# Performance work log

Hardware: AMD Instinct MI355X
Metric: run time of the kernel (lower is better)

Reference implementation:

```python
import jax, jax.numpy as jnp
import numpy as np

B, T, V = 128, 1024, 192
EPS = 1e-8


def setup_inputs() -> dict:
    key = jax.random.key(0)
    k1, k2, k3, k4, k5 = jax.random.split(key, 5)
    return {
        "emissions": jax.random.normal(k1, (B, T, V), dtype=jnp.float32),
        "tags": jax.random.randint(k2, (B, T), 0, V, dtype=jnp.int64),
        "mask": jnp.ones((B, T), dtype=jnp.int32),
        "transitions": jax.random.normal(k3, (V, V), dtype=jnp.float32) * 0.1,
        "start_trans": jax.random.normal(k4, (V,), dtype=jnp.float32) * 0.1,
        "end_trans": jax.random.normal(k5, (V,), dtype=jnp.float32) * 0.1,
    }


def _lse(x, axis):
    # matches torch _log_sum_exp: max + log(sum(exp(x-max)) + 1e-8)
    m = jnp.max(x, axis=axis)
    return m + jnp.log(jnp.sum(jnp.exp(x - jnp.expand_dims(m, axis)), axis=axis) + EPS)


def _log_partition(emissions, mask, transitions, start_trans, end_trans):
    # emissions: (B,T,V), mask: (B,T) int
    alpha0 = start_trans[None, :] + emissions[:, 0, :]  # (B,V)
    em_t = jnp.moveaxis(emissions[:, 1:, :], 1, 0)       # (T-1,B,V)
    mk_t = jnp.moveaxis(mask[:, 1:], 1, 0).astype(bool)  # (T-1,B)

    def step(alpha, inp):
        emit, m = inp  # (B,V), (B,)
        # (B, V_prev, V_next)
        scores = alpha[:, :, None] + transitions[None, :, :] + emit[:, None, :]
        new_alpha = _lse(scores, axis=1)
        alpha = jnp.where(m[:, None], new_alpha, alpha)
        return alpha, None

    alpha, _ = jax.lax.scan(step, alpha0, (em_t, mk_t))
    return _lse(alpha + end_trans[None, :], axis=1)  # (B,)


def _gold_score(emissions, tags, mask, transitions, start_trans, end_trans):
    Bq, Tq, _ = emissions.shape
    maskf = mask.astype(emissions.dtype)
    # emission score of gold tags at each step: (B,T)
    emit = jnp.take_along_axis(emissions, tags[:, :, None], axis=2)[:, :, 0]
    # transitions between consecutive gold tags: (B,T-1)
    trans = transitions[tags[:, :-1], tags[:, 1:]]
    score = start_trans[tags[:, 0]] + emit[:, 0]
    score = score + jnp.sum((emit[:, 1:] + trans) * maskf[:, 1:], axis=1)
    last_idx = jnp.sum(mask, axis=1).astype(jnp.int32) - 1  # (B,)
    last_tags = jnp.take_along_axis(tags, last_idx[:, None].astype(tags.dtype), axis=1)[:, 0]
    score = score + end_trans[last_tags]
    return score


def reference(emissions, tags, mask, transitions, start_trans, end_trans):
    log_den = _log_partition(emissions, mask, transitions, start_trans, end_trans)
    log_num = _gold_score(emissions, tags, mask, transitions, start_trans, end_trans)
    raw_loss = log_den - log_num
    seq_len = jnp.clip(jnp.sum(mask, axis=1).astype(emissions.dtype), 1.0)
    return raw_loss / seq_len  # (B,)
```

## Files before the change

kernel.cpp:

```cpp
#include <hip/hip_runtime.h>

#define BB 128
#define TT 1024
#define VV 192
#define NTHREADS 256
#define NWAVES 4
#define LN2 0.69314718055994530942f
#define WS_STRIDE 448

typedef int   intx8   __attribute__((ext_vector_type(8)));
typedef float floatx2 __attribute__((ext_vector_type(2)));
typedef float floatx4 __attribute__((ext_vector_type(4)));

__device__ __forceinline__ float bf8_to_f32(unsigned char h) {
    floatx2 v = __builtin_amdgcn_cvt_pk_f32_bf8((int)(unsigned int)h, false);
    return v.x;
}
__device__ __forceinline__ unsigned char f32_to_bf8(float f) {
    int pk = __builtin_amdgcn_cvt_pk_bf8_f32(f, f, 0, false);
    return (unsigned char)(pk & 0xff);
}
__device__ __forceinline__ unsigned char f32_to_fp8(float f) {
    int pk = __builtin_amdgcn_cvt_pk_fp8_f32(f, f, 0, false);
    return (unsigned char)(pk & 0xff);
}

#define LBAR() __asm__ volatile("s_waitcnt lgkmcnt(0)\n\ts_barrier" ::: "memory")

template<int DIR>
__device__ __forceinline__ void crf_body(const float* __restrict__ emissions,
                                         const int* __restrict__ tags,
                                         const int* __restrict__ mask,
                                         const float* __restrict__ trans,
                                         const float* __restrict__ start_trans,
                                         const float* __restrict__ end_trans,
                                         float* __restrict__ ws)
{
    const int b = blockIdx.x;
    const int tid = threadIdx.x;
    const int lane = tid & 63;
    const int wid = tid >> 6;
    const int quad = lane >> 4;
    const int col = lane & 15;

    __shared__ __align__(16) unsigned char qpad[2][256];
    __shared__ unsigned int smaskp[33];
    __shared__ float wg[NWAVES];
    __shared__ float wsl[NWAVES];

    const float* em_b = emissions + (size_t)b * TT * VV;
    const int* mask_b = mask + b * TT;
    float* wsb = ws + (size_t)b * WS_STRIDE;

    const int nl = wid * 48 + (quad < 3 ? quad : 0) * 16 + col;

    #define ROWOF(u) (DIR ? (TT - 1 - (u)) : (u))

    intx8 ef[6];
    #pragma unroll
    for (int kt = 0; kt < 2; ++kt) {
        #pragma unroll
        for (int h = 0; h < 3; ++h) {
            const int n = wid * 48 + h * 16 + col;
            intx8 v;
            #pragma unroll
            for (int w = 0; w < 8; ++w) {
                unsigned int word = 0;
                #pragma unroll
                for (int by = 0; by < 4; ++by) {
                    int k = kt * 128 + quad * 32 + w * 4 + by;
                    float x = (k < VV) ? __expf(trans[DIR ? (k + n * VV) : (k * VV + n)]) : 0.f;
                    word |= (unsigned int)f32_to_fp8(x) << (8 * by);
                }
                v[w] = (int)word;
            }
            ef[kt * 3 + h] = v;
        }
    }

    for (int i = tid; i < 512; i += NTHREADS) ((unsigned char*)qpad)[i] = 0;

    if (tid < 33) {
        if (tid == 32) smaskp[32] = 0u;
        else {
            unsigned int m = 0;
            #pragma unroll 4
            for (int j = 0; j < 32; ++j) m |= (mask_b[tid * 32 + j] ? 1u : 0u) << j;
            smaskp[tid] = m;
        }
    }

    float em0[8], em1[8];
    #pragma unroll
    for (int r = 0; r < 8; ++r) em0[r] = em_b[(size_t)ROWOF(r) * VV + nl];
    #pragma unroll
    for (int r = 0; r < 8; ++r) em1[r] = em_b[(size_t)ROWOF(8 + r) * VV + nl];
    float em_fin = em_b[(size_t)ROWOF(512) * VV + nl];

    __syncthreads();
    if (tid < VV) {
        float a0 = DIR ? (end_trans[tid] + em_b[(size_t)(TT - 1) * VV + tid])
                       : (start_trans[tid] + em_b[tid]);
        qpad[0][tid] = f32_to_bf8(fminf(__expf(a0), 28672.f));
    }
    float carry2 = 0.f;
    int cur = 0;
    float peprev = __expf(em0[0]);
    __syncthreads();

    unsigned long long mk64 = 0; int boff = 0;
    auto fetchwin = [&](int u0w) {
        int wbase = DIR ? (TT - u0w - 16) : u0w;
        int mw = wbase >> 5;
        unsigned mlo = (unsigned)__builtin_amdgcn_readfirstlane((int)smaskp[mw]);
        unsigned mhi = (unsigned)__builtin_amdgcn_readfirstlane((int)smaskp[mw + 1]);
        mk64 = (((unsigned long long)mhi) << 32) | (unsigned long long)mlo;
        boff = wbase & 31;
    };
    auto getmk = [&](int i) -> int {
        int sh = DIR ? (boff + 16 - i) : (boff + i);
        return (int)((mk64 >> sh) & 1ull);
    };

    auto dostep = [&](float emraw, int mk) {
        unsigned char* qc = qpad[cur];
        const intx8* qv = (const intx8*)qc;
        intx8 A0 = qv[quad];
        intx8 A1 = qv[quad + 4];
        unsigned char prevb = 0;
        if (!mk) prevb = qc[nl];

        floatx4 aA[3], aB[3];
        #pragma unroll
        for (int h = 0; h < 3; ++h) { aA[h] = (floatx4){0.f,0.f,0.f,0.f};
                                      aB[h] = (floatx4){0.f,0.f,0.f,0.f}; }
        #pragma unroll
        for (int h = 0; h < 3; ++h)
            aA[h] = __builtin_amdgcn_mfma_scale_f32_16x16x128_f8f6f4(
                        A0, ef[h], aA[h], 1, 0, 0, 0x7f7f7f7f, 0, 0x7f7f7f7f);
        #pragma unroll
        for (int h = 0; h < 3; ++h)
            aB[h] = __builtin_amdgcn_mfma_scale_f32_16x16x128_f8f6f4(
                        A1, ef[3 + h], aB[h], 1, 0, 0, 0x7f7f7f7f, 0, 0x7f7f7f7f);

        int q0i = __builtin_amdgcn_readfirstlane(A0[0]);
        float q0 = bf8_to_f32((unsigned char)(q0i & 0xff));
        float r = __builtin_amdgcn_rcpf(q0);
        carry2 += mk ? __log2f(q0) : 0.f;
        float pe = __expf(emraw);
        float sc = pe * r;

        float s0 = aA[0][0] + aB[0][0];
        float s1 = aA[1][0] + aB[1][0];
        float s2 = aA[2][0] + aB[2][0];
        float v = (quad == 1) ? s1 : ((quad == 2) ? s2 : s0);
        float qn = fminf(v * sc, 28672.f);
        unsigned char nb;
        if (mk) {
            nb = f32_to_bf8(qn);
        } else {
            nb = DIR ? f32_to_bf8(fminf(bf8_to_f32(prevb) * pe *
                                        __builtin_amdgcn_rcpf(peprev), 28672.f))
                     : prevb;
        }
        qpad[cur ^ 1][nl] = nb;
        LBAR();
        cur ^= 1;
        if (DIR) peprev = pe;
    };

    for (int u0 = 0; u0 < 496; u0 += 16) {
        fetchwin(u0);
        if (u0 > 0) dostep(em0[0], getmk(0));
        dostep(em0[1], getmk(1));
        dostep(em0[2], getmk(2));
        dostep(em0[3], getmk(3));
        dostep(em0[4], getmk(4));
        dostep(em0[5], getmk(5));
        dostep(em0[6], getmk(6));
        dostep(em0[7], getmk(7));
        {
            #pragma unroll
            for (int r = 0; r < 8; ++r) {
                int rr = u0 + 16 + r;
                em0[r] = em_b[(size_t)ROWOF(rr) * VV + nl];
            }
        }
        dostep(em1[0], getmk(8));
        dostep(em1[1], getmk(9));
        dostep(em1[2], getmk(10));
        dostep(em1[3], getmk(11));
        dostep(em1[4], getmk(12));
        dostep(em1[5], getmk(13));
        dostep(em1[6], getmk(14));
        dostep(em1[7], getmk(15));
        {
            #pragma unroll
            for (int r = 0; r < 8; ++r) {
                int rr = u0 + 24 + r;
                em1[r] = em_b[(size_t)ROWOF(rr) * VV + nl];
            }
        }
    }
    fetchwin(496);
    dostep(em0[0], getmk(0)); dostep(em0[1], getmk(1));
    dostep(em0[2], getmk(2)); dostep(em0[3], getmk(3));
    dostep(em0[4], getmk(4)); dostep(em0[5], getmk(5));
    dostep(em0[6], getmk(6)); dostep(em0[7], getmk(7));
    dostep(em1[0], getmk(8)); dostep(em1[1], getmk(9));
    dostep(em1[2], getmk(10)); dostep(em1[3], getmk(11));
    dostep(em1[4], getmk(12)); dostep(em1[5], getmk(13));
    dostep(em1[6], getmk(14));

    if (DIR == 0) {
        dostep(em1[7], getmk(15));
        dostep(em_fin, getmk(16));
        if (tid < VV) wsb[tid] = bf8_to_f32(qpad[cur][tid]);
    } else {
        unsigned char* qc = qpad[cur];
        const intx8* qv = (const intx8*)qc;
        intx8 A0 = qv[quad];
        intx8 A1 = qv[quad + 4];
        int mk = (int)((smaskp[513 >> 5] >> (513 & 31)) & 1u);
        floatx4 aA[3], aB[3];
        #pragma unroll
        for (int h = 0; h < 3; ++h) { aA[h] = (floatx4){0.f,0.f,0.f,0.f};
                                      aB[h] = (floatx4){0.f,0.f,0.f,0.f}; }
        #pragma unroll
        for (int h = 0; h < 3; ++h)
            aA[h] = __builtin_amdgcn_mfma_scale_f32_16x16x128_f8f6f4(
                        A0, ef[h], aA[h], 1, 0, 0, 0x7f7f7f7f, 0, 0x7f7f7f7f);
        #pragma unroll
        for (int h = 0; h < 3; ++h)
            aB[h] = __builtin_amdgcn_mfma_scale_f32_16x16x128_f8f6f4(
                        A1, ef[3 + h], aB[h], 1, 0, 0, 0x7f7f7f7f, 0, 0x7f7f7f7f);
        if (quad < 3) {
            float s0 = aA[0][0] + aB[0][0];
            float s1 = aA[1][0] + aB[1][0];
            float s2 = aA[2][0] + aB[2][0];
            float v = (quad == 1) ? s1 : ((quad == 2) ? s2 : s0);
            if (!mk) v = bf8_to_f32(qc[nl]) * __builtin_amdgcn_rcpf(peprev);
            wsb[192 + nl] = v;
        }
    }
    if (tid == 0) wsb[384 + DIR] = carry2;

    float gp = 0.f;
    float sl = 0.f;
    for (int t = tid; t < TT; t += NTHREADS) {
        int mk = (int)((smaskp[t >> 5] >> (t & 31)) & 1u);
        bool inS = DIR ? (t >= 512) : (t < 512);
        if (inS) sl += (float)mk;
        bool inG = DIR ? (t >= 513) : (t >= 1 && t <= 512);
        if (inG) {
            int tg  = tags[b * TT + t];
            int tgp = tags[b * TT + t - 1];
            float term = em_b[(size_t)t * VV + tg] + trans[tgp * VV + tg];
            gp += mk ? term : 0.f;
        }
    }
    #pragma unroll
    for (int off = 1; off < 64; off <<= 1) {
        gp += __shfl_xor(gp, off);
        sl += __shfl_xor(sl, off);
    }
    if (lane == 0) { wg[wid] = gp; wsl[wid] = sl; }
    __syncthreads();
    if (tid == 0) {
        float g = 0.f, s = 0.f;
        for (int w = 0; w < NWAVES; ++w) { g += wg[w]; s += wsl[w]; }
        if (DIR == 0) {
            int tg0 = tags[b * TT];
            g += start_trans[tg0] + em_b[tg0];
        }
        wsb[386 + DIR] = g;
        wsb[388 + DIR] = s;
    }
    #undef ROWOF
}

__launch_bounds__(NTHREADS, 1)
__global__ void crf_half_kernel(const float* __restrict__ emissions,
                                const int* __restrict__ tags,
                                const int* __restrict__ mask,
                                const float* __restrict__ trans,
                                const float* __restrict__ start_trans,
                                const float* __restrict__ end_trans,
                                float* __restrict__ ws)
{
    if (blockIdx.y == 0)
        crf_body<0>(emissions, tags, mask, trans, start_trans, end_trans, ws);
    else
        crf_body<1>(emissions, tags, mask, trans, start_trans, end_trans, ws);
}

__global__ void crf_combine(const float* __restrict__ ws,
                            const int* __restrict__ tags,
                            const float* __restrict__ end_trans,
                            float* __restrict__ out)
{
    const int b = blockIdx.x;
    const int lane = threadIdx.x;
    const float* wsb = ws + (size_t)b * WS_STRIDE;
    float s = 0.f;
    #pragma unroll
    for (int i = lane; i < VV; i += 64) s += wsb[i] * wsb[192 + i];
    #pragma unroll
    for (int off = 1; off < 64; off <<= 1) s += __shfl_xor(s, off);
    if (lane == 0) {
        float logden = LN2 * (wsb[384] + wsb[385]) + __logf(s + 1e-8f);
        float gold = wsb[386] + wsb[387];
        int seqs = (int)(wsb[388] + wsb[389]);
        int last_idx = seqs - 1; if (last_idx < 0) last_idx = 0;
        gold += end_trans[tags[b * TT + last_idx]];
        float seqf = fmaxf((float)seqs, 1.0f);
        out[b] = (logden - gold) / seqf;
    }
}

extern "C" void kernel_launch(void* const* d_in, const int* in_sizes, int n_in,
                              void* d_out, int out_size, void* d_ws, size_t ws_size,
                              hipStream_t stream) {
    const float* emissions   = (const float*)d_in[0];
    const int*   tags        = (const int*)d_in[1];
    const int*   mask        = (const int*)d_in[2];
    const float* trans       = (const float*)d_in[3];
    const float* start_trans = (const float*)d_in[4];
    const float* end_trans   = (const float*)d_in[5];
    float* out = (float*)d_out;
    float* ws  = (float*)d_ws;

    crf_half_kernel<<<dim3(BB, 2), NTHREADS, 0, stream>>>(emissions, tags, mask, trans,
                                                          start_trans, end_trans, ws);
    crf_combine<<<BB, 64, 0, stream>>>(ws, tags, end_trans, out);
}
```

Baseline: 292.0 us.

## Split each half-sequence scan into four concurrent chunks with burn-in for ILP

Each 512-step directional scan is split into four chunks that run interleaved in one block. Chunks after the first start from a uniform vector and run a short burn-in, and the normalized state after burn-in is used to recover each chunk's log-scale contribution. This cuts the serial dependency chain from about 512 steps to about 144 rounds, with four independent MFMA chains per round hiding latency. In exchange each round does four times the work and shared memory, and the result relies on the forward-algorithm state forgetting its start (mixing) within the burn-in window, which is only approximately exact.

```diff
diff --git a/kernel.cpp b/kernel.cpp
--- a/kernel.cpp
+++ b/kernel.cpp
@@ -4,7 +4,6 @@
 #define TT 1024
 #define VV 192
 #define NTHREADS 256
-#define NWAVES 4
 #define LN2 0.69314718055994530942f
 #define WS_STRIDE 448
 
@@ -43,10 +42,9 @@
     const int quad = lane >> 4;
     const int col = lane & 15;
 
-    __shared__ __align__(16) unsigned char qpad[2][256];
+    __shared__ __align__(16) unsigned char qpad[4][2][256];
     __shared__ unsigned int smaskp[33];
-    __shared__ float wg[NWAVES];
-    __shared__ float wsl[NWAVES];
+    __shared__ float wgs[4], wsls[4];
 
     const float* em_b = emissions + (size_t)b * TT * VV;
     const int* mask_b = mask + b * TT;
@@ -54,7 +52,11 @@
 
     const int nl = wid * 48 + (quad < 3 ? quad : 0) * 16 + col;
 
-    #define ROWOF(u) (DIR ? (TT - 1 - (u)) : (u))
+    const int firstc[4] = {1, 113, 241, DIR ? 367 : 369};
+    const int capRc[4]  = {0, 16, 16, DIR ? 18 : 16};
+    const int capPc[4]  = {128, 144, 144, 0};
+
+    #define ROW_OF(x) (DIR ? (TT - 1 - (x)) : (x))
 
     intx8 ef[6];
     #pragma unroll
@@ -78,7 +80,7 @@
         }
     }
 
-    for (int i = tid; i < 512; i += NTHREADS) ((unsigned char*)qpad)[i] = 0;
+    for (int i = tid; i < 4 * 512; i += NTHREADS) ((unsigned char*)qpad)[i] = 0;
 
     if (tid < 33) {
         if (tid == 32) smaskp[32] = 0u;
@@ -90,163 +92,176 @@
         }
     }
 
-    float em0[8], em1[8];
-    #pragma unroll
-    for (int r = 0; r < 8; ++r) em0[r] = em_b[(size_t)ROWOF(r) * VV + nl];
-    #pragma unroll
-    for (int r = 0; r < 8; ++r) em1[r] = em_b[(size_t)ROWOF(8 + r) * VV + nl];
-    float em_fin = em_b[(size_t)ROWOF(512) * VV + nl];
+    float em0[4][8], em1[4][8];
+    #pragma unroll
+    for (int c = 0; c < 4; ++c) {
+        #pragma unroll
+        for (int r = 0; r < 8; ++r) em0[c][r] = em_b[(size_t)ROW_OF(firstc[c] + r) * VV + nl];
+        #pragma unroll
+        for (int r = 0; r < 8; ++r) em1[c][r] = em_b[(size_t)ROW_OF(firstc[c] + 8 + r) * VV + nl];
+    }
+    float pep[4] = {0.f, 0.f, 0.f, 0.f};
+    if (DIR) {
+        #pragma unroll
+        for (int c = 0; c < 4; ++c)
+            pep[c] = __expf(em_b[(size_t)ROW_OF(firstc[c] - 1) * VV + nl]);
+    }
 
     __syncthreads();
     if (tid < VV) {
         float a0 = DIR ? (end_trans[tid] + em_b[(size_t)(TT - 1) * VV + tid])
                        : (start_trans[tid] + em_b[tid]);
-        qpad[0][tid] = f32_to_bf8(fminf(__expf(a0), 28672.f));
-    }
-    float carry2 = 0.f;
+        qpad[0][0][tid] = f32_to_bf8(fminf(__expf(a0), 28672.f));
+        unsigned char one = f32_to_bf8(1.0f);
+        qpad[1][0][tid] = one;
+        qpad[2][0][tid] = one;
+        qpad[3][0][tid] = one;
+    }
+    float carry[4] = {0.f,0.f,0.f,0.f}, Rv[4] = {0.f,0.f,0.f,0.f};
+    float Pv[4] = {0.f,0.f,0.f,0.f}, csv[4] = {0.f,0.f,0.f,0.f};
     int cur = 0;
-    float peprev = __expf(em0[0]);
     __syncthreads();
 
-    unsigned long long mk64 = 0; int boff = 0;
-    auto fetchwin = [&](int u0w) {
-        int wbase = DIR ? (TT - u0w - 16) : u0w;
-        int mw = wbase >> 5;
-        unsigned mlo = (unsigned)__builtin_amdgcn_readfirstlane((int)smaskp[mw]);
-        unsigned mhi = (unsigned)__builtin_amdgcn_readfirstlane((int)smaskp[mw + 1]);
-        mk64 = (((unsigned long long)mhi) << 32) | (unsigned long long)mlo;
-        boff = wbase & 31;
-    };
-    auto getmk = [&](int i) -> int {
-        int sh = DIR ? (boff + 16 - i) : (boff + i);
-        return (int)((mk64 >> sh) & 1ull);
-    };
-
-    auto dostep = [&](float emraw, int mk) {
-        unsigned char* qc = qpad[cur];
-        const intx8* qv = (const intx8*)qc;
+    unsigned long long mk64[4];
+    int shb[4];
+
+#define GETMK(c, I) ((int)((mk64[c] >> (DIR ? (shb[c] + 15 - (I)) : (shb[c] + (I)))) & 1ull))
+
+#define ROUND(I)                                                               \
+    {                                                                          \
+        intx8 a0_[4], a1_[4];                                                  \
+        _Pragma("unroll")                                                      \
+        for (int c = 0; c < 4; ++c) {                                          \
+            const intx8* qv = (const intx8*)qpad[c][cur];                      \
+            a0_[c] = qv[quad];                                                 \
+            a1_[c] = qv[quad + 4];                                             \
+        }                                                                      \
+        floatx4 aA_[4][3], aB_[4][3];                                          \
+        _Pragma("unroll")                                                      \
+        for (int c = 0; c < 4; ++c) {                                          \
+            _Pragma("unroll")                                                  \
+            for (int h = 0; h < 3; ++h) {                                      \
+                floatx4 z = (floatx4){0.f, 0.f, 0.f, 0.f};                     \
+                aA_[c][h] = __builtin_amdgcn_mfma_scale_f32_16x16x128_f8f6f4(  \
+                    a0_[c], ef[h], z, 1, 0, 0, 0x7f7f7f7f, 0, 0x7f7f7f7f);     \
+                aB_[c][h] = __builtin_amdgcn_mfma_scale_f32_16x16x128_f8f6f4(  \
+                    a1_[c], ef[3 + h], z, 1, 0, 0, 0x7f7f7f7f, 0, 0x7f7f7f7f); \
+            }                                                                  \
+        }                                                                      \
+        _Pragma("unroll")                                                      \
+        for (int c = 0; c < 4; ++c) {                                          \
+            int mk = GETMK(c, I);                                              \
+            unsigned char prevb = 0;                                           \
+            if (!mk) prevb = qpad[c][cur][nl];                                 \
+            int q0i = __builtin_amdgcn_readfirstlane(a0_[c][0]);               \
+            float q0 = bf8_to_f32((unsigned char)(q0i & 0xff));                \
+            float rr = __builtin_amdgcn_rcpf(q0);                              \
+            carry[c] += mk ? __log2f(q0) : 0.f;                                \
+            float emraw = ((I) < 8) ? em0[c][(I) & 7] : em1[c][(I) & 7];       \
+            float pe = __expf(emraw);                                          \
+            float sc = pe * rr;                                                \
+            float s0 = aA_[c][0][0] + aB_[c][0][0];                            \
+            float s1 = aA_[c][1][0] + aB_[c][1][0];                            \
+            float s2 = aA_[c][2][0] + aB_[c][2][0];                            \
+            float vv = (quad == 1) ? s1 : ((quad == 2) ? s2 : s0);             \
+            float qn = fminf(vv * sc, 28672.f);                                \
+            unsigned char nb;                                                  \
+            if (mk) nb = f32_to_bf8(qn);                                       \
+            else nb = DIR ? f32_to_bf8(fminf(bf8_to_f32(prevb) * pe *          \
+                                 __builtin_amdgcn_rcpf(pep[c]), 28672.f))      \
+                          : prevb;                                             \
+            qpad[c][cur ^ 1][nl] = nb;                                         \
+            if (DIR) pep[c] = pe;                                              \
+        }                                                                      \
+        LBAR();                                                                \
+        cur ^= 1;                                                              \
+        {                                                                      \
+            int L = lb + (I) + 1;                                              \
+            _Pragma("unroll")                                                  \
+            for (int c = 0; c < 4; ++c) {                                      \
+                if (L == capRc[c]) {                                           \
+                    Rv[c] = __log2f(bf8_to_f32(qpad[c][cur][0]));              \
+                    carry[c] = 0.f;                                            \
+                }                                                              \
+                if (L == capPc[c]) {                                           \
+                    Pv[c] = __log2f(bf8_to_f32(qpad[c][cur][0]));              \
+                    csv[c] = carry[c];                                         \
+                }                                                              \
+            }                                                                  \
+        }                                                                      \
+    }
+
+    for (int w = 0; w < 9; ++w) {
+        const int lb = 16 * w;
+        #pragma unroll
+        for (int c = 0; c < 4; ++c) {
+            int gw = firstc[c] + lb;
+            int base = DIR ? (1024 - gw - 15) : gw;
+            unsigned lo = (unsigned)__builtin_amdgcn_readfirstlane((int)smaskp[base >> 5]);
+            unsigned hi = (unsigned)__builtin_amdgcn_readfirstlane((int)smaskp[(base >> 5) + 1]);
+            mk64[c] = (((unsigned long long)hi) << 32) | (unsigned long long)lo;
+            shb[c] = base & 31;
+        }
+        ROUND(0) ROUND(1) ROUND(2) ROUND(3)
+        ROUND(4) ROUND(5) ROUND(6) ROUND(7)
+        {
+            #pragma unroll
+            for (int c = 0; c < 4; ++c) {
+                #pragma unroll
+                for (int r = 0; r < 8; ++r)
+                    em0[c][r] = em_b[(size_t)ROW_OF(firstc[c] + lb + 16 + r) * VV + nl];
+            }
+        }
+        ROUND(8) ROUND(9) ROUND(10) ROUND(11)
+        ROUND(12) ROUND(13) ROUND(14) ROUND(15)
+        {
+            #pragma unroll
+            for (int c = 0; c < 4; ++c) {
+                #pragma unroll
+                for (int r = 0; r < 8; ++r)
+                    em1[c][r] = em_b[(size_t)ROW_OF(firstc[c] + lb + 24 + r) * VV + nl];
+            }
+        }
+    }
+#undef ROUND
+#undef GETMK
+
+    csv[3] = carry[3];
+
+    if (DIR == 0) {
+        if (tid < VV) wsb[tid] = bf8_to_f32(qpad[3][cur][tid]);
+    } else {
+        const intx8* qv = (const intx8*)qpad[3][cur];
         intx8 A0 = qv[quad];
         intx8 A1 = qv[quad + 4];
-        unsigned char prevb = 0;
-        if (!mk) prevb = qc[nl];
-
+        int mkf = (int)((smaskp[513 >> 5] >> (513 & 31)) & 1u);
         floatx4 aA[3], aB[3];
         #pragma unroll
-        for (int h = 0; h < 3; ++h) { aA[h] = (floatx4){0.f,0.f,0.f,0.f};
-                                      aB[h] = (floatx4){0.f,0.f,0.f,0.f}; }
-        #pragma unroll
-        for (int h = 0; h < 3; ++h)
+        for (int h = 0; h < 3; ++h) {
+            floatx4 z = (floatx4){0.f, 0.f, 0.f, 0.f};
             aA[h] = __builtin_amdgcn_mfma_scale_f32_16x16x128_f8f6f4(
-                        A0, ef[h], aA[h], 1, 0, 0, 0x7f7f7f7f, 0, 0x7f7f7f7f);
-        #pragma unroll
-        for (int h = 0; h < 3; ++h)
+                        A0, ef[h], z, 1, 0, 0, 0x7f7f7f7f, 0, 0x7f7f7f7f);
             aB[h] = __builtin_amdgcn_mfma_scale_f32_16x16x128_f8f6f4(
-                        A1, ef[3 + h], aB[h], 1, 0, 0, 0x7f7f7f7f, 0, 0x7f7f7f7f);
-
-        int q0i = __builtin_amdgcn_readfirstlane(A0[0]);
-        float q0 = bf8_to_f32((unsigned char)(q0i & 0xff));
-        float r = __builtin_amdgcn_rcpf(q0);
-        carry2 += mk ? __log2f(q0) : 0.f;
-        float pe = __expf(emraw);
-        float sc = pe * r;
-
-        float s0 = aA[0][0] + aB[0][0];
-        float s1 = aA[1][0] + aB[1][0];
-        float s2 = aA[2][0] + aB[2][0];
-        float v = (quad == 1) ? s1 : ((quad == 2) ? s2 : s0);
-        float qn = fminf(v * sc, 28672.f);
-        unsigned char nb;
-        if (mk) {
-            nb = f32_to_bf8(qn);
-        } else {
-            nb = DIR ? f32_to_bf8(fminf(bf8_to_f32(prevb) * pe *
-                                        __builtin_amdgcn_rcpf(peprev), 28672.f))
-                     : prevb;
-        }
-        qpad[cur ^ 1][nl] = nb;
-        LBAR();
-        cur ^= 1;
-        if (DIR) peprev = pe;
-    };
-
-    for (int u0 = 0; u0 < 496; u0 += 16) {
-        fetchwin(u0);
-        if (u0 > 0) dostep(em0[0], getmk(0));
-        dostep(em0[1], getmk(1));
-        dostep(em0[2], getmk(2));
-        dostep(em0[3], getmk(3));
-        dostep(em0[4], getmk(4));
-        dostep(em0[5], getmk(5));
-        dostep(em0[6], getmk(6));
-        dostep(em0[7], getmk(7));
-        {
-            #pragma unroll
-            for (int r = 0; r < 8; ++r) {
-                int rr = u0 + 16 + r;
-                em0[r] = em_b[(size_t)ROWOF(rr) * VV + nl];
-            }
-        }
-        dostep(em1[0], getmk(8));
-        dostep(em1[1], getmk(9));
-        dostep(em1[2], getmk(10));
-        dostep(em1[3], getmk(11));
-        dostep(em1[4], getmk(12));
-        dostep(em1[5], getmk(13));
-        dostep(em1[6], getmk(14));
-        dostep(em1[7], getmk(15));
-        {
-            #pragma unroll
-            for (int r = 0; r < 8; ++r) {
-                int rr = u0 + 24 + r;
-                em1[r] = em_b[(size_t)ROWOF(rr) * VV + nl];
-            }
-        }
-    }
-    fetchwin(496);
-    dostep(em0[0], getmk(0)); dostep(em0[1], getmk(1));
-    dostep(em0[2], getmk(2)); dostep(em0[3], getmk(3));
-    dostep(em0[4], getmk(4)); dostep(em0[5], getmk(5));
-    dostep(em0[6], getmk(6)); dostep(em0[7], getmk(7));
-    dostep(em1[0], getmk(8)); dostep(em1[1], getmk(9));
-    dostep(em1[2], getmk(10)); dostep(em1[3], getmk(11));
-    dostep(em1[4], getmk(12)); dostep(em1[5], getmk(13));
-    dostep(em1[6], getmk(14));
-
-    if (DIR == 0) {
-        dostep(em1[7], getmk(15));
-        dostep(em_fin, getmk(16));
-        if (tid < VV) wsb[tid] = bf8_to_f32(qpad[cur][tid]);
-    } else {
-        unsigned char* qc = qpad[cur];
-        const intx8* qv = (const intx8*)qc;
-        intx8 A0 = qv[quad];
-        intx8 A1 = qv[quad + 4];
-        int mk = (int)((smaskp[513 >> 5] >> (513 & 31)) & 1u);
-        floatx4 aA[3], aB[3];
-        #pragma unroll
-        for (int h = 0; h < 3; ++h) { aA[h] = (floatx4){0.f,0.f,0.f,0.f};
-                                      aB[h] = (floatx4){0.f,0.f,0.f,0.f}; }
-        #pragma unroll
-        for (int h = 0; h < 3; ++h)
-            aA[h] = __builtin_amdgcn_mfma_scale_f32_16x16x128_f8f6f4(
-                        A0, ef[h], aA[h], 1, 0, 0, 0x7f7f7f7f, 0, 0x7f7f7f7f);
-        #pragma unroll
-        for (int h = 0; h < 3; ++h)
-            aB[h] = __builtin_amdgcn_mfma_scale_f32_16x16x128_f8f6f4(
-                        A1, ef[3 + h], aB[h], 1, 0, 0, 0x7f7f7f7f, 0, 0x7f7f7f7f);
+                        A1, ef[3 + h], z, 1, 0, 0, 0x7f7f7f7f, 0, 0x7f7f7f7f);
+        }
         if (quad < 3) {
             float s0 = aA[0][0] + aB[0][0];
             float s1 = aA[1][0] + aB[1][0];
             float s2 = aA[2][0] + aB[2][0];
-            float v = (quad == 1) ? s1 : ((quad == 2) ? s2 : s0);
-            if (!mk) v = bf8_to_f32(qc[nl]) * __builtin_amdgcn_rcpf(peprev);
-            wsb[192 + nl] = v;
-        }
-    }
-    if (tid == 0) wsb[384 + DIR] = carry2;
-
-    float gp = 0.f;
-    float sl = 0.f;
+            float vv = (quad == 1) ? s1 : ((quad == 2) ? s2 : s0);
+            if (!mkf) vv = bf8_to_f32(qpad[3][cur][nl]) * __builtin_amdgcn_rcpf(pep[3]);
+            wsb[192 + nl] = vv;
+        }
+    }
+    if (tid == 0) {
+        #pragma unroll
+        for (int c = 0; c < 4; ++c) {
+            float contrib = csv[c] + ((c < 3) ? Pv[c] : 0.f) - ((c > 0) ? Rv[c] : 0.f);
+            wsb[384 + DIR * 8 + c] = contrib;
+        }
+    }
+
+    float gp = 0.f, sl = 0.f;
     for (int t = tid; t < TT; t += NTHREADS) {
         int mk = (int)((smaskp[t >> 5] >> (t & 31)) & 1u);
         bool inS = DIR ? (t >= 512) : (t < 512);
@@ -264,29 +279,29 @@
         gp += __shfl_xor(gp, off);
         sl += __shfl_xor(sl, off);
     }
-    if (lane == 0) { wg[wid] = gp; wsl[wid] = sl; }
+    if (lane == 0) { wgs[wid] = gp; wsls[wid] = sl; }
     __syncthreads();
     if (tid == 0) {
         float g = 0.f, s = 0.f;
-        for (int w = 0; w < NWAVES; ++w) { g += wg[w]; s += wsl[w]; }
+        for (int w = 0; w < 4; ++w) { g += wgs[w]; s += wsls[w]; }
         if (DIR == 0) {
             int tg0 = tags[b * TT];
             g += start_trans[tg0] + em_b[tg0];
         }
-        wsb[386 + DIR] = g;
-        wsb[388 + DIR] = s;
-    }
-    #undef ROWOF
+        wsb[384 + DIR * 8 + 4] = g;
+        wsb[384 + DIR * 8 + 5] = s;
+    }
+    #undef ROW_OF
 }
 
 __launch_bounds__(NTHREADS, 1)
-__global__ void crf_half_kernel(const float* __restrict__ emissions,
-                                const int* __restrict__ tags,
-                                const int* __restrict__ mask,
-                                const float* __restrict__ trans,
-                                const float* __restrict__ start_trans,
-                                const float* __restrict__ end_trans,
-                                float* __restrict__ ws)
+__global__ void crf_ilp_kernel(const float* __restrict__ emissions,
+                               const int* __restrict__ tags,
+                               const int* __restrict__ mask,
+                               const float* __restrict__ trans,
+                               const float* __restrict__ start_trans,
+                               const float* __restrict__ end_trans,
+                               float* __restrict__ ws)
 {
     if (blockIdx.y == 0)
         crf_body<0>(emissions, tags, mask, trans, start_trans, end_trans, ws);
@@ -308,9 +323,15 @@
     #pragma unroll
     for (int off = 1; off < 64; off <<= 1) s += __shfl_xor(s, off);
     if (lane == 0) {
-        float logden = LN2 * (wsb[384] + wsb[385]) + __logf(s + 1e-8f);
-        float gold = wsb[386] + wsb[387];
-        int seqs = (int)(wsb[388] + wsb[389]);
+        float T = 0.f, gold = 0.f, seq = 0.f;
+        for (int d = 0; d < 2; ++d) {
+            const float* slot = wsb + 384 + d * 8;
+            T    += slot[0] + slot[1] + slot[2] + slot[3];
+            gold += slot[4];
+            seq  += slot[5];
+        }
+        float logden = LN2 * T + __logf(s + 1e-8f);
+        int seqs = (int)(seq + 0.5f);
         int last_idx = seqs - 1; if (last_idx < 0) last_idx = 0;
         gold += end_trans[tags[b * TT + last_idx]];
         float seqf = fmaxf((float)seqs, 1.0f);
@@ -330,7 +351,7 @@
     float* out = (float*)d_out;
     float* ws  = (float*)d_ws;
 
-    crf_half_kernel<<<dim3(BB, 2), NTHREADS, 0, stream>>>(emissions, tags, mask, trans,
-                                                          start_trans, end_trans, ws);
+    crf_ilp_kernel<<<dim3(BB, 2), NTHREADS, 0, stream>>>(
+        emissions, tags, mask, trans, start_trans, end_trans, ws);
     crf_combine<<<BB, 64, 0, stream>>>(ws, tags, end_trans, out);
 }
```

New measurement: 409.9 us. 40.4% more time.
